# Kernel tuning notes

Hardware: AMD Instinct MI355X
Metric: run time of the kernel (lower is better)

Reference implementation:

```python
import jax, jax.numpy as jnp
import numpy as np

S, D, H, G, DH = 2048, 4096, 32, 8, 128  # seq, d_in, heads, kv_groups, head_dim
GROUP = H // G


def rotate_half(x):
    x1, x2 = jnp.split(x, 2, axis=-1)
    return jnp.concatenate([-x2, x1], axis=-1)


def setup_inputs() -> dict:
    key = jax.random.key(0)
    ks = jax.random.split(key, 8)
    x = jax.random.normal(ks[0], (1, S, D), dtype=jnp.float32)
    # causal mask: True above the diagonal (positions to mask out)
    mask = jnp.triu(jnp.ones((S, S), dtype=bool), k=1)
    # standard RoPE tables
    inv_freq = 1.0 / (10000.0 ** (np.arange(0, DH, 2, dtype=np.float32) / DH))
    t = np.arange(S, dtype=np.float32)
    freqs = np.outer(t, inv_freq)                      # [S, DH/2]
    emb = np.concatenate([freqs, freqs], axis=-1)      # [S, DH]
    cos = jnp.asarray(np.cos(emb), dtype=jnp.float32)
    sin = jnp.asarray(np.sin(emb), dtype=jnp.float32)
    sc = 0.02
    Wq = jax.random.normal(ks[1], (D, H * DH), dtype=jnp.float32) * sc
    Wk = jax.random.normal(ks[2], (D, G * DH), dtype=jnp.float32) * sc
    Wv = jax.random.normal(ks[3], (D, G * DH), dtype=jnp.float32) * sc
    Wo = jax.random.normal(ks[4], (H * DH, D), dtype=jnp.float32) * sc
    return {"x": x, "mask": mask, "cos": cos, "sin": sin,
            "Wq": Wq, "Wk": Wk, "Wv": Wv, "Wo": Wo}


def reference(x, mask, cos, sin, Wq, Wk, Wv, Wo):
    xs = x[0]                                          # [S, D] (batch must be 1)
    q = (xs @ Wq).reshape(S, H, DH).transpose(1, 0, 2)   # [H, S, DH]
    k = (xs @ Wk).reshape(S, G, DH).transpose(1, 0, 2)   # [G, S, DH]
    v = (xs @ Wv).reshape(S, G, DH).transpose(1, 0, 2)   # [G, S, DH]
    # RoPE
    q = q * cos[None] + rotate_half(q) * sin[None]
    k = k * cos[None] + rotate_half(k) * sin[None]
    # GQA: repeat KV groups to match query heads
    k = jnp.repeat(k, GROUP, axis=0)                   # [H, S, DH]
    v = jnp.repeat(v, GROUP, axis=0)                   # [H, S, DH]
    scores = jnp.einsum('hsd,htd->hst', q, k)          # [H, S, S]
    scores = jnp.where(mask[None], -jnp.inf, scores)
    scores = scores / jnp.sqrt(jnp.float32(DH))
    w = jax.nn.softmax(scores, axis=-1)
    ctx = jnp.einsum('hst,htd->hsd', w, v)             # [H, S, DH]
    ctx = ctx.transpose(1, 0, 2).reshape(S, H * DH)
    out = ctx @ Wo                                     # [S, D]
    return out[None]                                   # [1, S, D]
```

## Files before the change

kernel.cpp:

```cpp
#include <hip/hip_runtime.h>
#include <hip/hip_bf16.h>
#include <cstdint>
#include <cstddef>

#define S 2048
#define D 4096
#define H 32
#define G 8
#define DH 128
#define HD (H*DH)
#define GD (G*DH)

typedef __bf16 bf16;
typedef __bf16 bf16x4 __attribute__((ext_vector_type(4)));
typedef __bf16 bf16x8 __attribute__((ext_vector_type(8)));
typedef float f32x4 __attribute__((ext_vector_type(4)));

__device__ __forceinline__ void gload16(const void* g, void* l) {
    __builtin_amdgcn_global_load_lds(
        (const __attribute__((address_space(1))) void*)g,
        (__attribute__((address_space(3))) void*)l, 16, 0, 0);
}

#define FENCE() asm volatile("" ::: "memory")
#define BARRIER() do { FENCE(); __builtin_amdgcn_s_barrier(); FENCE(); } while (0)
#define VMCNT(n)  asm volatile("s_waitcnt vmcnt(" #n ")" ::: "memory")
#define LGKM0()   do { asm volatile("s_waitcnt lgkmcnt(0)" ::: "memory"); \
                       __builtin_amdgcn_sched_barrier(0); } while (0)

__global__ __launch_bounds__(256) void prep_fused(
    const float* __restrict__ x, bf16* __restrict__ xb,
    const float* __restrict__ Wq, const float* __restrict__ Wk,
    const float* __restrict__ Wv, bf16* __restrict__ Wqkvt)
{
    const int b = blockIdx.x, tid = threadIdx.x;
    if (b < 512) {
        int i = b * 4096 + tid;
        #pragma unroll
        for (int it = 0; it < 16; ++it, i += 256) {
            float4 v = reinterpret_cast<const float4*>(x)[i];
            bf16x4 o = { (bf16)v.x, (bf16)v.y, (bf16)v.z, (bf16)v.w };
            reinterpret_cast<bf16x4*>(xb)[i] = o;
        }
        return;
    }
    const float* in; bf16* out; int Cc, bx, by;
    if (b < 1536)      { int tb = b - 512;  in = Wq; out = Wqkvt;                       Cc = HD; bx = tb & 15; by = tb >> 4; }
    else if (b < 1792) { int tb = b - 1536; in = Wk; out = Wqkvt + (size_t)HD * D;      Cc = GD; bx = tb & 3;  by = tb >> 2; }
    else               { int tb = b - 1792; in = Wv; out = Wqkvt + (size_t)(HD+GD) * D; Cc = GD; bx = tb & 3;  by = tb >> 2; }
    const int r0 = by * 64 + (tid & 7) * 8;
    const int c0 = bx * 256 + (tid >> 3) * 8;
    bf16 m[8][8];
    #pragma unroll
    for (int j = 0; j < 8; ++j) {
        const float* p = in + (size_t)(r0 + j) * Cc + c0;
        float4 a = *reinterpret_cast<const float4*>(p);
        float4 bq = *reinterpret_cast<const float4*>(p + 4);
        m[j][0] = (bf16)a.x;  m[j][1] = (bf16)a.y;  m[j][2] = (bf16)a.z;  m[j][3] = (bf16)a.w;
        m[j][4] = (bf16)bq.x; m[j][5] = (bf16)bq.y; m[j][6] = (bf16)bq.z; m[j][7] = (bf16)bq.w;
    }
    #pragma unroll
    for (int i = 0; i < 8; ++i) {
        bf16x8 ov;
        #pragma unroll
        for (int j = 0; j < 8; ++j) ov[j] = m[j][i];
        *reinterpret_cast<bf16x8*>(out + (size_t)(c0 + i) * D + r0) = ov;
    }
}

__global__ __launch_bounds__(256) void rope_vt_fused(
    bf16* __restrict__ Qb, bf16* __restrict__ Kb,
    const bf16* __restrict__ Vb, bf16* __restrict__ VtG,
    const float* __restrict__ cosT, const float* __restrict__ sinT, float qs)
{
    const int b = blockIdx.x, tid = threadIdx.x;
    if (b < 20480) {
        bf16* Y; int ncols, idx; float scale;
        if (b < 16384) { Y = Qb; ncols = HD; idx = b * 256 + tid;           scale = qs; }
        else           { Y = Kb; ncols = GD; idx = (b - 16384) * 256 + tid; scale = 1.0f; }
        int pairs = ncols >> 1;
        int s = idx / pairs;
        int p = idx - s * pairs;
        int head = p >> 6;
        int d = p & 63;
        size_t base = (size_t)s * ncols + head * DH;
        float c  = cosT[s * DH + d];
        float sn = sinT[s * DH + d];
        float a = (float)Y[base + d];
        float bb = (float)Y[base + d + 64];
        Y[base + d]      = (bf16)((a * c - bb * sn) * scale);
        Y[base + d + 64] = (bf16)((bb * c + a * sn) * scale);
        return;
    }
    const int tb = b - 20480;
    const int r0 = (tb >> 2) * 64 + (tid & 7) * 8;
    const int c0 = (tb & 3) * 256 + (tid >> 3) * 8;
    bf16 m[8][8];
    #pragma unroll
    for (int j = 0; j < 8; ++j) {
        bf16x8 v = *reinterpret_cast<const bf16x8*>(Vb + (size_t)(r0 + j) * GD + c0);
        #pragma unroll
        for (int i = 0; i < 8; ++i) m[j][i] = v[i];
    }
    #pragma unroll
    for (int i = 0; i < 8; ++i) {
        bf16x8 ov;
        #pragma unroll
        for (int j = 0; j < 8; ++j) ov[j] = m[j][i];
        *reinterpret_cast<bf16x8*>(VtG + (size_t)(c0 + i) * S + r0) = ov;
    }
}

__global__ __launch_bounds__(256) void cast_f32_bf16(const float* __restrict__ in,
                                                     bf16* __restrict__ out, int n4)
{
    int i = blockIdx.x * 256 + threadIdx.x;
    if (i < n4) {
        float4 v = reinterpret_cast<const float4*>(in)[i];
        bf16x4 o = { (bf16)v.x, (bf16)v.y, (bf16)v.z, (bf16)v.w };
        reinterpret_cast<bf16x4*>(out)[i] = o;
    }
}

template<bool IN_F32>
__global__ __launch_bounds__(256) void transpose_to_bf16(
    const void* __restrict__ in, bf16* __restrict__ out, int R, int C)
{
    const int r0 = blockIdx.y * 64 + (threadIdx.x & 7) * 8;
    const int c0 = blockIdx.x * 256 + (threadIdx.x >> 3) * 8;
    bf16 m[8][8];
    #pragma unroll
    for (int j = 0; j < 8; ++j) {
        if constexpr (IN_F32) {
            const float* p = (const float*)in + (size_t)(r0 + j) * C + c0;
            float4 a = *reinterpret_cast<const float4*>(p);
            float4 b = *reinterpret_cast<const float4*>(p + 4);
            m[j][0] = (bf16)a.x; m[j][1] = (bf16)a.y; m[j][2] = (bf16)a.z; m[j][3] = (bf16)a.w;
            m[j][4] = (bf16)b.x; m[j][5] = (bf16)b.y; m[j][6] = (bf16)b.z; m[j][7] = (bf16)b.w;
        } else {
            const bf16* p = (const bf16*)in + (size_t)(r0 + j) * C + c0;
            bf16x8 v = *reinterpret_cast<const bf16x8*>(p);
            #pragma unroll
            for (int i = 0; i < 8; ++i) m[j][i] = v[i];
        }
    }
    #pragma unroll
    for (int i = 0; i < 8; ++i) {
        bf16x8 ov;
        #pragma unroll
        for (int j = 0; j < 8; ++j) ov[j] = m[j][i];
        *reinterpret_cast<bf16x8*>(out + (size_t)(c0 + i) * R + r0) = ov;
    }
}

__global__ __launch_bounds__(256) void rope_inplace(bf16* __restrict__ Y,
                                                    const float* __restrict__ cosT,
                                                    const float* __restrict__ sinT,
                                                    int ncols, int total, float scale)
{
    int idx = blockIdx.x * 256 + threadIdx.x;
    if (idx >= total) return;
    int pairs = ncols >> 1;
    int s = idx / pairs;
    int p = idx - s * pairs;
    int head = p >> 6;
    int d = p & 63;
    size_t base = (size_t)s * ncols + head * DH;
    float c  = cosT[s * DH + d];
    float sn = sinT[s * DH + d];
    float a = (float)Y[base + d];
    float b = (float)Y[base + d + 64];
    Y[base + d]      = (bf16)((a * c - b * sn) * scale);
    Y[base + d + 64] = (bf16)((b * c + a * sn) * scale);
}

__global__ __launch_bounds__(512) void gemm8p(
    const bf16* __restrict__ A, const bf16* __restrict__ Bt,
    bf16* __restrict__ Qout, bf16* __restrict__ Kout, bf16* __restrict__ Vout,
    const float* __restrict__ WoIn, bf16* __restrict__ WotOut,
    int N, int K, int ngemm)
{
    extern __shared__ char smem[];
    const int tid = threadIdx.x;

    if ((int)blockIdx.x >= ngemm) {
        const int tb = blockIdx.x - ngemm;
        const int r0 = tb * 64 + (tid & 7) * 8;
        #pragma unroll 1
        for (int pass = 0; pass < 8; ++pass) {
            const int c0 = pass * 512 + (tid >> 3) * 8;
            bf16 m[8][8];
            #pragma unroll
            for (int j = 0; j < 8; ++j) {
                const float* p = WoIn + (size_t)(r0 + j) * D + c0;
                float4 a = *reinterpret_cast<const float4*>(p);
                float4 b = *reinterpret_cast<const float4*>(p + 4);
                m[j][0] = (bf16)a.x; m[j][1] = (bf16)a.y; m[j][2] = (bf16)a.z; m[j][3] = (bf16)a.w;
                m[j][4] = (bf16)b.x; m[j][5] = (bf16)b.y; m[j][6] = (bf16)b.z; m[j][7] = (bf16)b.w;
            }
            #pragma unroll
            for (int i = 0; i < 8; ++i) {
                bf16x8 ov;
                #pragma unroll
                for (int j = 0; j < 8; ++j) ov[j] = m[j][i];
                *reinterpret_cast<bf16x8*>(WotOut + (size_t)(c0 + i) * HD + r0) = ov;
            }
        }
        return;
    }

    const int lane = tid & 63, wave = tid >> 6;
    const int wr = wave >> 2, wc = wave & 3;
    const int l15 = lane & 15, lhi = lane >> 4;
    const int r8 = lane >> 3, c8 = lane & 7;
    const int csw = ((c8 ^ r8) << 3);

    const int x = blockIdx.x & 7, i = blockIdx.x >> 3;
    const int brow = (x >> 2) * 4 + (i & 3);
    const int bcol = (x & 3) * 6 + (i >> 2);
    const int bm = brow * 256, bn = bcol * 256;
    const int NT = K >> 6;

    auto stageA = [&](int buf, int h, int t) {
        #pragma unroll
        for (int L = 0; L < 2; ++L) {
            int row0 = L * 128 + h * 64 + wave * 8;
            gload16(A + (size_t)(bm + row0 + r8) * K + (t << 6) + csw,
                    smem + buf * 65536 + row0 * 128);
        }
    };
    auto stageB = [&](int buf, int h, int t) {
        #pragma unroll
        for (int L = 0; L < 2; ++L) {
            int row0 = h * 128 + L * 64 + wave * 8;
            gload16(Bt + (size_t)(bn + row0 + r8) * K + (t << 6) + csw,
                    smem + buf * 65536 + 32768 + row0 * 128);
        }
    };
    auto rdA = [&](const char* Ab, int mh, int ks, bf16x8* af) {
        #pragma unroll
        for (int m = 0; m < 4; ++m) {
            int row = wr * 128 + mh * 64 + m * 16 + l15;
            int ch = (ks * 4 + lhi) ^ (l15 & 7);
            af[m] = *reinterpret_cast<const bf16x8*>(Ab + row * 128 + ch * 16);
        }
    };
    auto rdB = [&](const char* Bb, int ks, bf16x8* bfv) {
        #pragma unroll
        for (int n = 0; n < 4; ++n) {
            int row = wc * 64 + n * 16 + l15;
            int ch = (ks * 4 + lhi) ^ (l15 & 7);
            bfv[n] = *reinterpret_cast<const bf16x8*>(Bb + row * 128 + ch * 16);
        }
    };

    f32x4 acc[8][4] = {};

    auto mm = [&](int mh, const bf16x8* af, const bf16x8* bfv) {
        LGKM0();
        __builtin_amdgcn_s_setprio(1);
        #pragma unroll
        for (int m = 0; m < 4; ++m)
            #pragma unroll
            for (int n = 0; n < 4; ++n)
                acc[mh * 4 + m][n] = __builtin_amdgcn_mfma_f32_16x16x32_bf16(
                    af[m], bfv[n], acc[mh * 4 + m][n], 0, 0, 0);
        __builtin_amdgcn_s_setprio(0);
    };

    stageA(0, 0, 0); stageA(0, 1, 0); stageB(0, 0, 0); stageB(0, 1, 0);
    stageA(1, 0, 1);
    VMCNT(2);
    BARRIER();

    const char* A0 = smem;
    const char* B0 = smem + 32768;
    const char* A1 = smem + 65536;
    const char* B1 = smem + 65536 + 32768;

    for (int j = 0; j < (NT >> 1); ++j) {
        const int tb = 2 * j + 1;
        const int t2 = (2 * j + 2 < NT) ? 2 * j + 2 : NT - 1;
        const int t3 = (2 * j + 3 < NT) ? 2 * j + 3 : NT - 1;
        bf16x8 af[4], bk0[4], bk1[4];

        rdB(B0, 0, bk0); rdA(A0, 0, 0, af);
        stageA(1, 1, tb);
        mm(0, af, bk0);
        BARRIER();

        rdB(B0, 1, bk1); rdA(A0, 0, 1, af);
        stageB(1, 0, tb);
        mm(0, af, bk1);
        BARRIER();

        rdA(A0, 1, 0, af);
        stageB(1, 1, tb);
        mm(1, af, bk0);
        BARRIER();

        rdA(A0, 1, 1, af);
        stageA(0, 0, t2);
        mm(1, af, bk1);
        VMCNT(2);
        BARRIER();

        rdB(B1, 0, bk0); rdA(A1, 0, 0, af);
        stageA(0, 1, t2);
        mm(0, af, bk0);
        BARRIER();

        rdB(B1, 1, bk1); rdA(A1, 0, 1, af);
        stageB(0, 0, t2);
        mm(0, af, bk1);
        BARRIER();

        rdA(A1, 1, 0, af);
        stageB(0, 1, t2);
        mm(1, af, bk0);
        BARRIER();

        rdA(A1, 1, 1, af);
        stageA(1, 0, t3);
        mm(1, af, bk1);
        VMCNT(2);
        BARRIER();
    }

    #pragma unroll
    for (int m = 0; m < 8; ++m) {
        int r0 = bm + wr * 128 + m * 16 + lhi * 4;
        #pragma unroll
        for (int n = 0; n < 4; ++n) {
            int c = bn + wc * 64 + n * 16 + l15;
            #pragma unroll
            for (int j = 0; j < 4; ++j) {
                bf16 v = (bf16)acc[m][n][j];
                if (bn < HD)
                    Qout[(size_t)(r0 + j) * HD + c] = v;
                else if (bn < HD + GD)
                    Kout[(size_t)(r0 + j) * GD + (c - HD)] = v;
                else
                    Vout[(size_t)(r0 + j) * GD + (c - HD - GD)] = v;
            }
        }
    }
}

__global__ __launch_bounds__(512, 2) void gemm3b(
    const bf16* __restrict__ A, const bf16* __restrict__ Bt,
    float* __restrict__ C, int N, int K)
{
    extern __shared__ char smem[];
    const int tid = threadIdx.x, lane = tid & 63, wave = tid >> 6;
    const int wr = wave >> 1, wc = wave & 1;
    const int l15 = lane & 15, lhi = lane >> 4;
    const int r8 = lane >> 3, c8 = lane & 7;
    const int csw = ((c8 ^ r8) << 3);

    const int x = blockIdx.x & 7, i = blockIdx.x >> 3;
    const int brow = (x >> 2) * 4 + (i & 3);
    const int bcol = (x & 3) * 8 + (i >> 2);
    const int bm = brow * 256, bn = bcol * 128;
    const int NT = K >> 6;

    auto stageA = [&](int buf, int L, int t) {
        int row0 = L * 64 + wave * 8;
        gload16(A + (size_t)(bm + row0 + r8) * K + (t << 6) + csw,
                smem + buf * 49152 + row0 * 128);
    };
    auto stageB = [&](int buf, int L, int t) {
        int row0 = L * 64 + wave * 8;
        gload16(Bt + (size_t)(bn + row0 + r8) * K + (t << 6) + csw,
                smem + buf * 49152 + 32768 + row0 * 128);
    };
    auto rdA = [&](const char* Ab, int ks, bf16x8* af) {
        #pragma unroll
        for (int m = 0; m < 4; ++m) {
            int row = wr * 64 + m * 16 + l15;
            int ch = (ks * 4 + lhi) ^ (l15 & 7);
            af[m] = *reinterpret_cast<const bf16x8*>(Ab + row * 128 + ch * 16);
        }
    };
    auto rdB = [&](const char* Bb, int ks, bf16x8* bfv) {
        #pragma unroll
        for (int n = 0; n < 4; ++n) {
            int row = wc * 64 + n * 16 + l15;
            int ch = (ks * 4 + lhi) ^ (l15 & 7);
            bfv[n] = *reinterpret_cast<const bf16x8*>(Bb + row * 128 + ch * 16);
        }
    };

    f32x4 acc[4][4] = {};

    #pragma unroll
    for (int L = 0; L < 4; ++L) stageA(0, L, 0);
    stageB(0, 0, 0); stageB(0, 1, 0);
    #pragma unroll
    for (int L = 0; L < 4; ++L) stageA(1, L, (1 < NT) ? 1 : 0);
    stageB(1, 0, (1 < NT) ? 1 : 0); stageB(1, 1, (1 < NT) ? 1 : 0);
    VMCNT(6);
    BARRIER();

    for (int t = 0; t < NT; ++t) {
        const char* Ab = smem + (t % 3) * 49152;
        const char* Bb = Ab + 32768;
        const int b2 = (t + 2) % 3;
        const int st = (t + 2 < NT) ? t + 2 : NT - 1;
        bf16x8 af[4], bk[4];

        rdB(Bb, 0, bk); rdA(Ab, 0, af);
        stageA(b2, 0, st); stageA(b2, 1, st);
        LGKM0();
        __builtin_amdgcn_s_setprio(1);
        #pragma unroll
        for (int m = 0; m < 4; ++m)
            #pragma unroll
            for (int n = 0; n < 4; ++n)
                acc[m][n] = __builtin_amdgcn_mfma_f32_16x16x32_bf16(af[m], bk[n], acc[m][n], 0, 0, 0);
        __builtin_amdgcn_s_setprio(0);

        rdB(Bb, 1, bk); rdA(Ab, 1, af);
        stageA(b2, 2, st); stageA(b2, 3, st);
        stageB(b2, 0, st); stageB(b2, 1, st);
        LGKM0();
        __builtin_amdgcn_s_setprio(1);
        #pragma unroll
        for (int m = 0; m < 4; ++m)
            #pragma unroll
            for (int n = 0; n < 4; ++n)
                acc[m][n] = __builtin_amdgcn_mfma_f32_16x16x32_bf16(af[m], bk[n], acc[m][n], 0, 0, 0);
        __builtin_amdgcn_s_setprio(0);

        VMCNT(6);
        BARRIER();
    }

    #pragma unroll
    for (int m = 0; m < 4; ++m) {
        int r0 = bm + wr * 64 + m * 16 + lhi * 4;
        #pragma unroll
        for (int n = 0; n < 4; ++n) {
            int c = bn + wc * 64 + n * 16 + l15;
            #pragma unroll
            for (int j = 0; j < 4; ++j)
                C[(size_t)(r0 + j) * N + c] = acc[m][n][j];
        }
    }
}

#define BM 128
#define BN 128
#define BK 32
#define LDSK 40

template<bool OUT_BF16>
__global__ __launch_bounds__(256) void gemm_aBf16(
    const bf16* __restrict__ A,
    const float* __restrict__ B0, const float* __restrict__ B1,
    void* __restrict__ C0, void* __restrict__ C1,
    int M, int N, int K)
{
    __shared__ alignas(16) bf16 Al[BM][LDSK];
    __shared__ alignas(16) bf16 Bt[BN][LDSK];

    const float* __restrict__ B = blockIdx.z ? B1 : B0;
    void* __restrict__ C = blockIdx.z ? C1 : C0;

    const int tid  = threadIdx.x;
    const int lane = tid & 63;
    const int wave = tid >> 6;
    const int wm = (wave >> 1) * 64;
    const int wn = (wave & 1) * 64;
    const int bm = blockIdx.y * BM;
    const int bn = blockIdx.x * BN;
    const int l15 = lane & 15;
    const int lhi = lane >> 4;

    f32x4 acc[4][4] = {};

    for (int k0 = 0; k0 < K; k0 += BK) {
        #pragma unroll
        for (int it = 0; it < 2; ++it) {
            int idx = it * 256 + tid;
            int row = idx >> 2;
            int ko  = idx & 3;
            bf16x8 v = *reinterpret_cast<const bf16x8*>(
                A + (size_t)(bm + row) * K + k0 + ko * 8);
            *reinterpret_cast<bf16x8*>(&Al[row][ko * 8]) = v;
        }
        {
            int n = tid & 127;
            int kbase = (tid >> 7) * 8;
            const float* bp = B + (size_t)k0 * N + bn + n;
            #pragma unroll
            for (int half = 0; half < 2; ++half) {
                bf16x8 v;
                #pragma unroll
                for (int j = 0; j < 8; ++j)
                    v[j] = (bf16)bp[(size_t)(half * 16 + kbase + j) * N];
                *reinterpret_cast<bf16x8*>(&Bt[n][half * 16 + kbase]) = v;
            }
        }
        __syncthreads();

        bf16x8 af[4], bfv[4];
        #pragma unroll
        for (int m = 0; m < 4; ++m)
            af[m] = *reinterpret_cast<const bf16x8*>(&Al[wm + m * 16 + l15][lhi * 8]);
        #pragma unroll
        for (int n = 0; n < 4; ++n)
            bfv[n] = *reinterpret_cast<const bf16x8*>(&Bt[wn + n * 16 + l15][lhi * 8]);
        #pragma unroll
        for (int m = 0; m < 4; ++m)
            #pragma unroll
            for (int n = 0; n < 4; ++n)
                acc[m][n] = __builtin_amdgcn_mfma_f32_16x16x32_bf16(
                    af[m], bfv[n], acc[m][n], 0, 0, 0);
        __syncthreads();
    }

    #pragma unroll
    for (int m = 0; m < 4; ++m) {
        int r0 = bm + wm + m * 16 + lhi * 4;
        #pragma unroll
        for (int n = 0; n < 4; ++n) {
            int c = bn + wn + n * 16 + l15;
            #pragma unroll
            for (int j = 0; j < 4; ++j) {
                if constexpr (OUT_BF16)
                    reinterpret_cast<bf16*>(C)[(size_t)(r0 + j) * N + c] = (bf16)acc[m][n][j];
                else
                    reinterpret_cast<float*>(C)[(size_t)(r0 + j) * N + c] = acc[m][n][j];
            }
        }
    }
}

#define QBLK 128
#define KVBLK 64
#define NQT (S/QBLK)

template<bool MASK>
__device__ __forceinline__ void attn_tile(
    int t0, int q0, int wave, int l15, int lhi,
    const bf16x8* qf, const char* Kl, const char* Vl, char* Plw,
    f32x4* o, float* m_i, float* l_i)
{
    f32x4 sc[4] = {};
    __builtin_amdgcn_s_setprio(1);
    #pragma unroll
    for (int n = 0; n < 4; ++n) {
        int row = n * 16 + l15;
        #pragma unroll
        for (int kk = 0; kk < 4; ++kk) {
            bf16x8 kf = *reinterpret_cast<const bf16x8*>(
                Kl + row * 256 + ((((kk * 4 + lhi)) ^ (l15 & 7)) << 4));
            sc[n] = __builtin_amdgcn_mfma_f32_16x16x32_bf16(qf[kk], kf, sc[n], 0, 0, 0);
        }
    }
    __builtin_amdgcn_s_setprio(0);

    float corr[4];
    #pragma unroll
    for (int j = 0; j < 4; ++j) {
        const int qr = q0 + wave * 16 + lhi * 4 + j;
        float vals[4];
        float mx = -1e30f;
        #pragma unroll
        for (int n = 0; n < 4; ++n) {
            float v = sc[n][j];
            if constexpr (MASK) {
                int t = t0 + n * 16 + l15;
                if (t > qr) v = -1e30f;
            }
            vals[n] = v;
            mx = fmaxf(mx, v);
        }
        #pragma unroll
        for (int ms = 1; ms < 16; ms <<= 1)
            mx = fmaxf(mx, __shfl_xor(mx, ms, 16));
        float mnew, cr;
        if (mx <= m_i[j] + 8.0f) { mnew = m_i[j]; cr = 1.0f; }
        else                     { mnew = mx; cr = exp2f(m_i[j] - mnew); }
        float rsum = 0.f;
        #pragma unroll
        for (int n = 0; n < 4; ++n) {
            float p = exp2f(vals[n] - mnew);
            rsum += p;
            int r = lhi * 4 + j;
            int off = ((r << 7) + ((n * 16 + l15) << 1)) ^ ((r & 7) << 4);
            *reinterpret_cast<bf16*>(Plw + off) = (bf16)p;
        }
        #pragma unroll
        for (int ms = 1; ms < 16; ms <<= 1)
            rsum += __shfl_xor(rsum, ms, 16);
        l_i[j] = l_i[j] * cr + rsum;
        m_i[j] = mnew;
        corr[j] = cr;
    }

    if ((corr[0] != 1.f) | (corr[1] != 1.f) | (corr[2] != 1.f) | (corr[3] != 1.f)) {
        #pragma unroll
        for (int n = 0; n < 8; ++n)
            #pragma unroll
            for (int j = 0; j < 4; ++j)
                o[n][j] *= corr[j];
    }

    __builtin_amdgcn_s_setprio(1);
    #pragma unroll
    for (int kk = 0; kk < 2; ++kk) {
        bf16x8 pf = *reinterpret_cast<const bf16x8*>(
            Plw + (l15 << 7) + ((((kk * 4 + lhi)) ^ (l15 & 7)) << 4));
        #pragma unroll
        for (int n = 0; n < 8; ++n) {
            int d = n * 16 + l15;
            bf16x8 vf = *reinterpret_cast<const bf16x8*>(
                Vl + (d << 7) + ((((kk * 4 + lhi)) ^ (d & 7)) << 4));
            o[n] = __builtin_amdgcn_mfma_f32_16x16x32_bf16(pf, vf, o[n], 0, 0, 0);
        }
    }
    __builtin_amdgcn_s_setprio(0);
}

__global__ __launch_bounds__(512) void flash_fwd5(
    const bf16* __restrict__ Q, const bf16* __restrict__ Kr,
    const bf16* __restrict__ VtG, bf16* __restrict__ ctx)
{
    extern __shared__ char fsm[];

    const int tid  = threadIdx.x;
    const int lane = tid & 63;
    const int wave = tid >> 6;
    const int l15 = lane & 15;
    const int lhi = lane >> 4;
    const int bid = blockIdx.x;
    const int qt = (NQT - 1) - (bid >> 5);
    const int h  = ((bid & 7) << 2) | ((bid >> 3) & 3);
    const int g  = h >> 2;
    const int q0 = qt * QBLK;
    char* Plw = fsm + 65536 + wave * 2048;

    bf16x8 qf[4];
    {
        const bf16* qp = Q + (size_t)(q0 + wave * 16 + l15) * HD + h * DH + lhi * 8;
        #pragma unroll
        for (int kk = 0; kk < 4; ++kk)
            qf[kk] = *reinterpret_cast<const bf16x8*>(qp + kk * 32);
    }

    f32x4 o[8] = {};
    float m_i[4] = { -1e30f, -1e30f, -1e30f, -1e30f };
    float l_i[4] = {};

    auto stage = [&](int t0, int buf) {
        char* Kl = fsm + buf * 32768;
        char* Vl = Kl + 16384;
        #pragma unroll
        for (int t = 0; t < 2; ++t) {
            int ch = t * 512 + tid;
            {
                int row = ch >> 4, ci = ch & 15;
                gload16(Kr + (size_t)(t0 + row) * GD + g * DH + ((ci ^ (row & 7)) << 3),
                        Kl + ch * 16);
            }
            {
                int d = ch >> 3, ci = ch & 7;
                gload16(VtG + (size_t)(g * DH + d) * S + t0 + ((ci ^ (d & 7)) << 3),
                        Vl + ch * 16);
            }
        }
    };

    const int nt = 2 * qt + 2;
    stage(0, 0);
    VMCNT(0);
    BARRIER();

    for (int it = 0; it < nt; ++it) {
        if (it + 1 < nt) stage((it + 1) * KVBLK, (it + 1) & 1);
        const char* Kl = fsm + (it & 1) * 32768;
        const char* Vl = Kl + 16384;
        if (it >= nt - 2)
            attn_tile<true>(it * KVBLK, q0, wave, l15, lhi, qf, Kl, Vl, Plw, o, m_i, l_i);
        else
            attn_tile<false>(it * KVBLK, q0, wave, l15, lhi, qf, Kl, Vl, Plw, o, m_i, l_i);
        VMCNT(0);
        BARRIER();
    }

    #pragma unroll
    for (int n = 0; n < 8; ++n) {
        int c = h * DH + n * 16 + l15;
        #pragma unroll
        for (int j = 0; j < 4; ++j) {
            int r = q0 + wave * 16 + lhi * 4 + j;
            ctx[(size_t)r * HD + c] = (bf16)(o[n][j] / l_i[j]);
        }
    }
}

extern "C" void kernel_launch(void* const* d_in, const int* in_sizes, int n_in,
                              void* d_out, int out_size, void* d_ws, size_t ws_size,
                              hipStream_t stream)
{
    const float* x    = (const float*)d_in[0];
    const float* cosT = (const float*)d_in[2];
    const float* sinT = (const float*)d_in[3];
    const float* Wq   = (const float*)d_in[4];
    const float* Wk   = (const float*)d_in[5];
    const float* Wv   = (const float*)d_in[6];
    const float* Wo   = (const float*)d_in[7];
    float* out = (float*)d_out;

    const size_t MB = (size_t)1 << 20;
    char* ws = (char*)d_ws;
    bf16* xb  = (bf16*)ws;
    bf16* ctx = (bf16*)(ws + 16 * MB);
    bf16* Qb  = (bf16*)d_out;
    bf16* Kb  = Qb + (size_t)S * HD;
    bf16* Vb  = Kb + (size_t)S * GD;
    bf16* VtG = Vb + (size_t)S * GD;

    const bool fast = ws_size >= 112 * MB;
    const float qscale = 0.08838834764831845f * 1.4426950408889634f;

    hipFuncSetAttribute(reinterpret_cast<const void*>(&flash_fwd5),
                        hipFuncAttributeMaxDynamicSharedMemorySize, 81920);

    if (fast) {
        bf16* Wqkvt = (bf16*)(ws + 32 * MB);
        bf16* Wot   = (bf16*)(ws + 80 * MB);

        hipFuncSetAttribute(reinterpret_cast<const void*>(&gemm8p),
                            hipFuncAttributeMaxDynamicSharedMemorySize, 131072);
        hipFuncSetAttribute(reinterpret_cast<const void*>(&gemm3b),
                            hipFuncAttributeMaxDynamicSharedMemorySize, 147456);

        prep_fused<<<2048, 256, 0, stream>>>(x, xb, Wq, Wk, Wv, Wqkvt);

        gemm8p<<<256, 512, 131072, stream>>>(
            xb, Wqkvt, Qb, Kb, Vb, Wo, Wot, HD + 2 * GD, D, 192);

        rope_vt_fused<<<20608, 256, 0, stream>>>(Qb, Kb, Vb, VtG, cosT, sinT, qscale);

        flash_fwd5<<<NQT * H, 512, 81920, stream>>>(Qb, Kb, VtG, ctx);

        gemm3b<<<256, 512, 147456, stream>>>(ctx, Wot, out, D, HD);
    } else {
        cast_f32_bf16<<<(S * D / 4 + 255) / 256, 256, 0, stream>>>(x, xb, S * D / 4);

        gemm_aBf16<true><<<dim3(HD / BN, S / BM, 1), 256, 0, stream>>>(
            xb, Wq, Wq, (void*)Qb, (void*)Qb, S, HD, D);
        gemm_aBf16<true><<<dim3(GD / BN, S / BM, 2), 256, 0, stream>>>(
            xb, Wk, Wv, (void*)Kb, (void*)Vb, S, GD, D);

        rope_inplace<<<(S * HD / 2 + 255) / 256, 256, 0, stream>>>(Qb, cosT, sinT, HD, S * HD / 2, qscale);
        rope_inplace<<<(S * GD / 2 + 255) / 256, 256, 0, stream>>>(Kb, cosT, sinT, GD, S * GD / 2, 1.0f);

        transpose_to_bf16<false><<<dim3(GD / 256, S / 64), 256, 0, stream>>>(Vb, VtG, S, GD);

        flash_fwd5<<<NQT * H, 512, 81920, stream>>>(Qb, Kb, VtG, ctx);

        gemm_aBf16<false><<<dim3(D / BN, S / BM, 1), 256, 0, stream>>>(
            ctx, Wo, Wo, (void*)out, (void*)out, S, D, HD);
    }

    (void)in_sizes; (void)n_in; (void)out_size; (void)ws_size;
}
```

Baseline: 336.2 us.

## Transpose QK^T MFMA so each lane owns one query row for softmax

Swaps the MFMA operand order in the score computation so the accumulator is S^T: each lane holds 16 scores for a single query row instead of 4 rows × 4 columns. Row max and row sum then become mostly in-register tree reductions plus two cross-lane shuffles, instead of 4 rows × 4 shuffle stages each. The running max and sum state shrinks to one scalar per lane, and P is written to LDS as packed bf16x4 vectors instead of scalar bf16 stores. Per-row correction factors and final normalisers now need extra shuffles to reach the output layout, and the swizzle used for the P writes must match the existing reads.

```diff
diff --git a/kernel.cpp b/kernel.cpp
--- a/kernel.cpp
+++ b/kernel.cpp
@@ -543,9 +543,9 @@
 
 template<bool MASK>
 __device__ __forceinline__ void attn_tile(
-    int t0, int q0, int wave, int l15, int lhi,
+    int t0, int q0w, int l15, int lhi,
     const bf16x8* qf, const char* Kl, const char* Vl, char* Plw,
-    f32x4* o, float* m_i, float* l_i)
+    f32x4* o, float& m_i, float& l_i)
 {
     f32x4 sc[4] = {};
     __builtin_amdgcn_s_setprio(1);
@@ -556,50 +556,61 @@
         for (int kk = 0; kk < 4; ++kk) {
             bf16x8 kf = *reinterpret_cast<const bf16x8*>(
                 Kl + row * 256 + ((((kk * 4 + lhi)) ^ (l15 & 7)) << 4));
-            sc[n] = __builtin_amdgcn_mfma_f32_16x16x32_bf16(qf[kk], kf, sc[n], 0, 0, 0);
+            sc[n] = __builtin_amdgcn_mfma_f32_16x16x32_bf16(kf, qf[kk], sc[n], 0, 0, 0);
         }
     }
     __builtin_amdgcn_s_setprio(0);
 
-    float corr[4];
-    #pragma unroll
-    for (int j = 0; j < 4; ++j) {
-        const int qr = q0 + wave * 16 + lhi * 4 + j;
-        float vals[4];
-        float mx = -1e30f;
-        #pragma unroll
-        for (int n = 0; n < 4; ++n) {
+    const int qr = q0w + l15;
+    float vals[16];
+    #pragma unroll
+    for (int n = 0; n < 4; ++n)
+        #pragma unroll
+        for (int j = 0; j < 4; ++j) {
             float v = sc[n][j];
             if constexpr (MASK) {
-                int t = t0 + n * 16 + l15;
+                int t = t0 + n * 16 + lhi * 4 + j;
                 if (t > qr) v = -1e30f;
             }
-            vals[n] = v;
-            mx = fmaxf(mx, v);
-        }
-        #pragma unroll
-        for (int ms = 1; ms < 16; ms <<= 1)
-            mx = fmaxf(mx, __shfl_xor(mx, ms, 16));
-        float mnew, cr;
-        if (mx <= m_i[j] + 8.0f) { mnew = m_i[j]; cr = 1.0f; }
-        else                     { mnew = mx; cr = exp2f(m_i[j] - mnew); }
-        float rsum = 0.f;
-        #pragma unroll
-        for (int n = 0; n < 4; ++n) {
-            float p = exp2f(vals[n] - mnew);
-            rsum += p;
-            int r = lhi * 4 + j;
-            int off = ((r << 7) + ((n * 16 + l15) << 1)) ^ ((r & 7) << 4);
-            *reinterpret_cast<bf16*>(Plw + off) = (bf16)p;
-        }
-        #pragma unroll
-        for (int ms = 1; ms < 16; ms <<= 1)
-            rsum += __shfl_xor(rsum, ms, 16);
-        l_i[j] = l_i[j] * cr + rsum;
-        m_i[j] = mnew;
-        corr[j] = cr;
-    }
-
+            vals[n * 4 + j] = v;
+        }
+
+    float m8[8], m4[4];
+    #pragma unroll
+    for (int k = 0; k < 8; ++k) m8[k] = fmaxf(vals[k], vals[k + 8]);
+    #pragma unroll
+    for (int k = 0; k < 4; ++k) m4[k] = fmaxf(m8[k], m8[k + 4]);
+    float mx = fmaxf(fmaxf(m4[0], m4[1]), fmaxf(m4[2], m4[3]));
+    mx = fmaxf(mx, __shfl_xor(mx, 16));
+    mx = fmaxf(mx, __shfl_xor(mx, 32));
+
+    const float mnew = (mx <= m_i + 8.0f) ? m_i : mx;
+    const float cr = exp2f(m_i - mnew);
+
+    float p[16];
+    #pragma unroll
+    for (int k = 0; k < 16; ++k) p[k] = exp2f(vals[k] - mnew);
+    float s8[8], s4[4];
+    #pragma unroll
+    for (int k = 0; k < 8; ++k) s8[k] = p[k] + p[k + 8];
+    #pragma unroll
+    for (int k = 0; k < 4; ++k) s4[k] = s8[k] + s8[k + 4];
+    float rsum = (s4[0] + s4[1]) + (s4[2] + s4[3]);
+    rsum += __shfl_xor(rsum, 16);
+    rsum += __shfl_xor(rsum, 32);
+    l_i = l_i * cr + rsum;
+    m_i = mnew;
+
+    #pragma unroll
+    for (int n = 0; n < 4; ++n) {
+        bf16x4 w = { (bf16)p[n*4+0], (bf16)p[n*4+1], (bf16)p[n*4+2], (bf16)p[n*4+3] };
+        int off = (l15 << 7) + (((n << 5) + (lhi << 3)) ^ ((l15 & 7) << 4));
+        *reinterpret_cast<bf16x4*>(Plw + off) = w;
+    }
+
+    float corr[4];
+    #pragma unroll
+    for (int j = 0; j < 4; ++j) corr[j] = __shfl(cr, lhi * 4 + j, 16);
     if ((corr[0] != 1.f) | (corr[1] != 1.f) | (corr[2] != 1.f) | (corr[3] != 1.f)) {
         #pragma unroll
         for (int n = 0; n < 8; ++n)
@@ -624,7 +635,7 @@
     __builtin_amdgcn_s_setprio(0);
 }
 
-__global__ __launch_bounds__(512) void flash_fwd5(
+__global__ __launch_bounds__(512) void flash_fwd6(
     const bf16* __restrict__ Q, const bf16* __restrict__ Kr,
     const bf16* __restrict__ VtG, bf16* __restrict__ ctx)
 {
@@ -640,19 +651,20 @@
     const int h  = ((bid & 7) << 2) | ((bid >> 3) & 3);
     const int g  = h >> 2;
     const int q0 = qt * QBLK;
+    const int q0w = q0 + wave * 16;
     char* Plw = fsm + 65536 + wave * 2048;
 
     bf16x8 qf[4];
     {
-        const bf16* qp = Q + (size_t)(q0 + wave * 16 + l15) * HD + h * DH + lhi * 8;
+        const bf16* qp = Q + (size_t)(q0w + l15) * HD + h * DH + lhi * 8;
         #pragma unroll
         for (int kk = 0; kk < 4; ++kk)
             qf[kk] = *reinterpret_cast<const bf16x8*>(qp + kk * 32);
     }
 
     f32x4 o[8] = {};
-    float m_i[4] = { -1e30f, -1e30f, -1e30f, -1e30f };
-    float l_i[4] = {};
+    float m_i = -1e30f;
+    float l_i = 0.f;
 
     auto stage = [&](int t0, int buf) {
         char* Kl = fsm + buf * 32768;
@@ -683,20 +695,24 @@
         const char* Kl = fsm + (it & 1) * 32768;
         const char* Vl = Kl + 16384;
         if (it >= nt - 2)
-            attn_tile<true>(it * KVBLK, q0, wave, l15, lhi, qf, Kl, Vl, Plw, o, m_i, l_i);
+            attn_tile<true>(it * KVBLK, q0w, l15, lhi, qf, Kl, Vl, Plw, o, m_i, l_i);
         else
-            attn_tile<false>(it * KVBLK, q0, wave, l15, lhi, qf, Kl, Vl, Plw, o, m_i, l_i);
+            attn_tile<false>(it * KVBLK, q0w, l15, lhi, qf, Kl, Vl, Plw, o, m_i, l_i);
         VMCNT(0);
         BARRIER();
     }
+
+    float lf[4];
+    #pragma unroll
+    for (int j = 0; j < 4; ++j) lf[j] = __shfl(l_i, lhi * 4 + j, 16);
 
     #pragma unroll
     for (int n = 0; n < 8; ++n) {
         int c = h * DH + n * 16 + l15;
         #pragma unroll
         for (int j = 0; j < 4; ++j) {
-            int r = q0 + wave * 16 + lhi * 4 + j;
-            ctx[(size_t)r * HD + c] = (bf16)(o[n][j] / l_i[j]);
+            int r = q0w + lhi * 4 + j;
+            ctx[(size_t)r * HD + c] = (bf16)(o[n][j] / lf[j]);
         }
     }
 }
@@ -726,7 +742,7 @@
     const bool fast = ws_size >= 112 * MB;
     const float qscale = 0.08838834764831845f * 1.4426950408889634f;
 
-    hipFuncSetAttribute(reinterpret_cast<const void*>(&flash_fwd5),
+    hipFuncSetAttribute(reinterpret_cast<const void*>(&flash_fwd6),
                         hipFuncAttributeMaxDynamicSharedMemorySize, 81920);
 
     if (fast) {
@@ -745,7 +761,7 @@
 
         rope_vt_fused<<<20608, 256, 0, stream>>>(Qb, Kb, Vb, VtG, cosT, sinT, qscale);
 
-        flash_fwd5<<<NQT * H, 512, 81920, stream>>>(Qb, Kb, VtG, ctx);
+        flash_fwd6<<<NQT * H, 512, 81920, stream>>>(Qb, Kb, VtG, ctx);
 
         gemm3b<<<256, 512, 147456, stream>>>(ctx, Wot, out, D, HD);
     } else {
@@ -761,7 +777,7 @@
 
         transpose_to_bf16<false><<<dim3(GD / 256, S / 64), 256, 0, stream>>>(Vb, VtG, S, GD);
 
-        flash_fwd5<<<NQT * H, 512, 81920, stream>>>(Qb, Kb, VtG, ctx);
+        flash_fwd6<<<NQT * H, 512, 81920, stream>>>(Qb, Kb, VtG, ctx);
 
         gemm_aBf16<false><<<dim3(D / BN, S / BM, 1), 256, 0, stream>>>(
             ctx, Wo, Wo, (void*)out, (void*)out, S, D, HD);
```

Result: faster. 319.0 us (-5.1%).
